# Kernel optimization log

Hardware: AMD Instinct MI355X
Metric: run time of the kernel (lower is better)

## Reference

```python
import jax, jax.numpy as jnp
import numpy as np

N_Q = 16384; N_S = 16384; NN = 32; F_IN = 128; F_OUT = 256
K = 15; DIM = 3
RADIUS = 10.0
KP_EXTENT_CFG = 1.0      # config.NETWORK.KP_EXTENT (also scales learned offsets)
DENSITY = 5.0            # config.NETWORK.DENSITY_PARAMETER
EXTENT = KP_EXTENT_CFG * RADIUS / DENSITY   # 2.0
K_RADIUS = 1.5 * EXTENT
OFFSET_DIM = DIM * (K - 1)  # modulated=False, version=0 -> 42


def setup_inputs() -> dict:
    key = jax.random.key(0)
    ks = jax.random.split(key, 8)
    query_points = jax.random.uniform(ks[0], (N_Q, DIM), dtype=jnp.float32)
    support_points = jax.random.uniform(ks[1], (N_S, DIM), dtype=jnp.float32)
    neighbors = jax.random.randint(ks[2], (N_Q, NN), 0, N_S)
    features = jax.random.normal(ks[3], (N_S, F_IN), dtype=jnp.float32)
    # kernel points: fixed disposition inside ball of radius 1.5*extent, first point at center
    kp = jax.random.normal(ks[4], (K, DIM), dtype=jnp.float32)
    kp = kp / jnp.linalg.norm(kp, axis=1, keepdims=True) * (0.7 * K_RADIUS)
    K_points = kp.at[0].set(0.0)
    weight = jax.random.normal(ks[5], (K, F_IN, F_OUT), dtype=jnp.float32) / np.sqrt(F_IN)
    deformable_weight = jax.random.normal(ks[6], (K, F_IN, OFFSET_DIM), dtype=jnp.float32) / np.sqrt(F_IN)
    bias = jnp.zeros((OFFSET_DIM,), dtype=jnp.float32)
    return {"query_points": query_points, "support_points": support_points,
            "neighbors": neighbors, "features": features, "K_points": K_points,
            "weight": weight, "deformable_weight": deformable_weight, "bias": bias}


def _gather_neighb(query_points, support_points, neighbors, features):
    # pad with shadow point (far away) and zero feature row, as in KPConv_ops
    sp = jnp.concatenate([support_points, jnp.full((1, DIM), 1e6, support_points.dtype)], 0)
    ft = jnp.concatenate([features, jnp.zeros((1, features.shape[1]), features.dtype)], 0)
    rel = sp[neighbors] - query_points[:, None, :]   # [n, nn, 3]
    nfeat = ft[neighbors]                            # [n, nn, f]
    return rel, nfeat


def _linear_influence(sq_dist):
    # KP_INFLUENCE='linear': relu(1 - d/extent); CONVOLUTION_MODE='sum'
    return jnp.maximum(1.0 - jnp.sqrt(sq_dist) / EXTENT, 0.0)


def reference(query_points, support_points, neighbors, features, K_points,
              weight, deformable_weight, bias):
    rel, nfeat = _gather_neighb(query_points, support_points, neighbors, features)

    # --- rigid KPConv producing offsets (version=0) ---
    d0 = rel[:, :, None, :] - K_points[None, None, :, :]   # [n, nn, K, 3]
    sq0 = jnp.sum(d0 * d0, axis=-1)                        # [n, nn, K]
    w0 = _linear_influence(sq0)
    wf0 = jnp.einsum('enk,enf->ekf', w0, nfeat)            # [n, K, f]
    feat0 = jnp.einsum('ekf,kfo->eo', wf0, deformable_weight) + bias  # [n, 42]

    # not modulated: reshape to offsets, prepend zero offset for center kernel point
    offsets = feat0.reshape(-1, K - 1, DIM)
    offsets = jnp.concatenate([jnp.zeros_like(offsets[:, :1, :]), offsets], axis=1)
    offsets = offsets * KP_EXTENT_CFG                      # [n, K, 3]

    # --- deformable KPConv ---
    def_kp = K_points[None, :, :] + offsets                # [n, K, 3]
    d1 = rel[:, :, None, :] - def_kp[:, None, :, :]        # [n, nn, K, 3]
    sq1 = jnp.sum(d1 * d1, axis=-1)                        # [n, nn, K]
    w1 = _linear_influence(sq1)                            # out-of-range neighbors get 0 weight
    wf1 = jnp.einsum('enk,enf->ekf', w1, nfeat)            # [n, K, f]
    out = jnp.einsum('ekf,kfo->eo', wf1, weight)           # [n, f_out]
    return out
```

## Files before the change

### kernel.cpp

```cpp
#include <hip/hip_runtime.h>
#include <hip/hip_bf16.h>
#include <math.h>

typedef __attribute__((ext_vector_type(8))) short bf16x8;
typedef __attribute__((ext_vector_type(4))) float f32x4;

#define NQ 16384
#define NN 32
#define FI 128
#define FO 256
#define KPN 15
#define OD 42
#define INV_EXT 0.5f

#define KT2 64
#define WST 2048

#define SWZ(row, blk) (((blk) ^ ((row) & 7)) << 5)

#define WS_FEATPK 0u
#define WS_BSW    (8u * 1024u * 1024u)
#define WS_DWBH   (9u * 1024u * 1024u)
#define WS_DWBL   (WS_DWBH + 196608u)
#define WS_DEFKP  (10u * 1024u * 1024u)

static __device__ __forceinline__ unsigned short f2bf(float x) {
    union { __hip_bfloat16 h; unsigned short u; } cv;
    cv.h = __float2bfloat16(x);
    return cv.u;
}
static __device__ __forceinline__ float bf2f(unsigned short h) {
    union { unsigned int u; float f; } cv;
    cv.u = ((unsigned int)h) << 16;
    return cv.f;
}

__global__ void pre_all(const float* __restrict__ feat, unsigned int* __restrict__ fpk,
                        const float* __restrict__ w, unsigned short* __restrict__ Bsw,
                        const float* __restrict__ dw,
                        unsigned short* __restrict__ dhi, unsigned short* __restrict__ dlo)
{
    const int b = blockIdx.x, t = threadIdx.x;
    if (b < 2048) {
        const int i = (b * 256 + t) * 4;
        float4 a = *(const float4*)&feat[i];
        unsigned short h0 = f2bf(a.x), h1 = f2bf(a.y), h2 = f2bf(a.z), h3 = f2bf(a.w);
        fpk[i + 0] = (unsigned int)h0 | ((unsigned int)f2bf(a.x - bf2f(h0)) << 16);
        fpk[i + 1] = (unsigned int)h1 | ((unsigned int)f2bf(a.y - bf2f(h1)) << 16);
        fpk[i + 2] = (unsigned int)h2 | ((unsigned int)f2bf(a.z - bf2f(h2)) << 16);
        fpk[i + 3] = (unsigned int)h3 | ((unsigned int)f2bf(a.w - bf2f(h3)) << 16);
    } else if (b < 2048 + 256) {
        const int tid = (b - 2048) * 256 + t;
        const int lane = tid & 63;
        const int kt   = (tid >> 6) & 63;
        const int nt   = tid >> 12;
        const int n    = nt * 16 + (lane & 15);
        const int kbase = kt * 32 + (lane >> 4) * 8;
        unsigned int p[4];
        #pragma unroll
        for (int jj = 0; jj < 4; jj++) {
            unsigned int lo, hi;
            {
                const int kk = kbase + 2 * jj;
                const int f = kk >> 4, k = kk & 15;
                lo = (k < KPN) ? f2bf(w[(k * FI + f) * FO + n]) : 0u;
            }
            {
                const int kk = kbase + 2 * jj + 1;
                const int f = kk >> 4, k = kk & 15;
                hi = (k < KPN) ? f2bf(w[(k * FI + f) * FO + n]) : 0u;
            }
            p[jj] = lo | (hi << 16);
        }
        unsigned int* op = (unsigned int*)&Bsw[tid * 8];
        op[0] = p[0]; op[1] = p[1]; op[2] = p[2]; op[3] = p[3];
    } else {
        const int tid = (b - 2304) * 256 + t;
        const int lane = tid & 63;
        const int kt   = (tid >> 6) & 63;
        const int nt   = tid >> 12;
        const int o    = nt * 16 + (lane & 15);
        const int kbase = kt * 32 + (lane >> 4) * 8;
        #pragma unroll
        for (int j = 0; j < 8; j++) {
            const int kf = kbase + j;
            const int f = kf >> 4, k = kf & 15;
            float v = (k < KPN && o < OD) ? dw[(k * FI + f) * OD + o] : 0.f;
            unsigned short h = f2bf(v);
            dhi[tid * 8 + j] = h;
            dlo[tid * 8 + j] = f2bf(v - bf2f(h));
        }
    }
}

__global__ __launch_bounds__(512, 4)
void k1_offsets(const float* __restrict__ query, const float* __restrict__ support,
                const int* __restrict__ neighbors, const unsigned int* __restrict__ featpk,
                const float* __restrict__ kpoints,
                const unsigned short* __restrict__ dwB_hi,
                const unsigned short* __restrict__ dwB_lo,
                const float* __restrict__ bias, float* __restrict__ defkp)
{
    __shared__ unsigned short wfA_hi[8 * WST];
    __shared__ unsigned short wfA_lo[8 * WST];
    __shared__ float relx[256], rely[256], relz[256];
    __shared__ int   nbr_s[256];
    __shared__ float kp_s[48];
    __shared__ f32x4 cred[3 * 64];

    const int t = threadIdx.x;
    const int qbase = blockIdx.x * 8;
    if (t < 45) kp_s[t] = kpoints[t];
    if (t >= 45 && t < 48) kp_s[t] = 0.f;

    if (t < 256) {
        const int e = t >> 5, n = t & 31;
        const int q = qbase + e;
        const int idx = neighbors[q * NN + n];
        nbr_s[t] = idx;
        relx[t] = support[idx * 3 + 0] - query[q * 3 + 0];
        rely[t] = support[idx * 3 + 1] - query[q * 3 + 1];
        relz[t] = support[idx * 3 + 2] - query[q * 3 + 2];
    }
    __syncthreads();

    const int wave = t >> 6, lane = t & 63;
    const int quad = lane >> 4, low = lane & 15;

    {
        const int ee = wave;
        const int kb = (low < KPN) ? low * 3 : 0;
        const float kx = kp_s[kb + 0], ky = kp_s[kb + 1], kz = kp_s[kb + 2];
        union { unsigned short u[8]; bf16x8 v; } ah, al;
        int rows[8];
        #pragma unroll
        for (int j = 0; j < 8; j++) {
            const int ni = ee * 32 + quad * 8 + j;
            rows[j] = nbr_s[ni];
            const float dx = relx[ni] - kx;
            const float dy = rely[ni] - ky;
            const float dz = relz[ni] - kz;
            const float d = sqrtf(dx * dx + dy * dy + dz * dz);
            float w = 1.0f - d * INV_EXT;
            w = (low < KPN && w > 0.f) ? w : 0.f;
            const unsigned short h = f2bf(w);
            ah.u[j] = h;
            al.u[j] = f2bf(w - bf2f(h));
        }
        #pragma unroll
        for (int ft = 0; ft < 8; ft++) {
            union { unsigned int u[4]; bf16x8 v; } bh, bl;
            #pragma unroll
            for (int jj = 0; jj < 4; jj++) {
                const unsigned int d0 = featpk[rows[2 * jj] * FI + ft * 16 + low];
                const unsigned int d1 = featpk[rows[2 * jj + 1] * FI + ft * 16 + low];
                bh.u[jj] = __builtin_amdgcn_perm(d1, d0, 0x05040100u);
                bl.u[jj] = __builtin_amdgcn_perm(d1, d0, 0x07060302u);
            }
            f32x4 acc = {0.f, 0.f, 0.f, 0.f};
            acc = __builtin_amdgcn_mfma_f32_16x16x32_bf16(al.v, bh.v, acc, 0, 0, 0);
            acc = __builtin_amdgcn_mfma_f32_16x16x32_bf16(ah.v, bl.v, acc, 0, 0, 0);
            acc = __builtin_amdgcn_mfma_f32_16x16x32_bf16(ah.v, bh.v, acc, 0, 0, 0);
            const int col  = ft * 16 + low;
            const int base = ee * WST + SWZ(ee, col >> 1) + ((col & 1) << 4) + quad * 4;
            const unsigned short h0 = f2bf(acc[0]), h1 = f2bf(acc[1]);
            const unsigned short h2 = f2bf(acc[2]), h3 = f2bf(acc[3]);
            unsigned int* ph = (unsigned int*)&wfA_hi[base];
            ph[0] = (unsigned int)h0 | ((unsigned int)h1 << 16);
            ph[1] = (unsigned int)h2 | ((unsigned int)h3 << 16);
            unsigned int* pl = (unsigned int*)&wfA_lo[base];
            pl[0] = (unsigned int)f2bf(acc[0] - bf2f(h0)) |
                    ((unsigned int)f2bf(acc[1] - bf2f(h1)) << 16);
            pl[1] = (unsigned int)f2bf(acc[2] - bf2f(h2)) |
                    ((unsigned int)f2bf(acc[3] - bf2f(h3)) << 16);
        }
    }
    __syncthreads();

    f32x4 acc = {0.f, 0.f, 0.f, 0.f};
    const int nt = wave >> 1, half = wave & 1;
    if (wave < 6) {
        const bf16x8* Bh = (const bf16x8*)dwB_hi;
        const bf16x8* Bl = (const bf16x8*)dwB_lo;
        const int rl = low & 7;
        const int arow = rl * WST;
        const int kt0 = half * 32;
        for (int kt = kt0; kt < kt0 + 32; kt++) {
            const int ao = arow + SWZ(rl, kt) + quad * 8;
            bf16x8 a_h = *(const bf16x8*)&wfA_hi[ao];
            bf16x8 a_l = *(const bf16x8*)&wfA_lo[ao];
            bf16x8 b_h = Bh[(nt * KT2 + kt) * 64 + lane];
            bf16x8 b_l = Bl[(nt * KT2 + kt) * 64 + lane];
            acc = __builtin_amdgcn_mfma_f32_16x16x32_bf16(a_l, b_h, acc, 0, 0, 0);
            acc = __builtin_amdgcn_mfma_f32_16x16x32_bf16(a_h, b_l, acc, 0, 0, 0);
            acc = __builtin_amdgcn_mfma_f32_16x16x32_bf16(a_h, b_h, acc, 0, 0, 0);
        }
        if (half == 1) cred[nt * 64 + lane] = acc;
    } else if (wave == 6 && lane < 24) {
        defkp[(qbase + lane / 3) * 45 + (lane % 3)] = kp_s[lane % 3];
    }
    __syncthreads();

    if (wave < 6 && half == 0) {
        f32x4 o2 = cred[nt * 64 + lane];
        acc[0] += o2[0]; acc[1] += o2[1]; acc[2] += o2[2]; acc[3] += o2[3];
        const int o = nt * 16 + low;
        if (quad < 2 && o < OD) {
            const float bo = bias[o] + kp_s[3 + o];
            #pragma unroll
            for (int r = 0; r < 4; r++) {
                const int ee = quad * 4 + r;
                defkp[(qbase + ee) * 45 + 3 + o] = bo + acc[r];
            }
        }
    }
}

__global__ __launch_bounds__(512, 4)
void k2_deform(const float* __restrict__ query, const float* __restrict__ support,
               const int* __restrict__ neighbors, const unsigned int* __restrict__ featpk,
               const unsigned short* __restrict__ Bsw, const float* __restrict__ defkp,
               float* __restrict__ out)
{
    __shared__ unsigned short wfA[16 * WST];
    __shared__ float relx[512], rely[512], relz[512];
    __shared__ float dk_s[16 * 45];
    __shared__ int   nbr_s[512];

    const int t = threadIdx.x;
    const int qbase = blockIdx.x * 16;

    for (int i = t; i < 16 * 45; i += 512) dk_s[i] = defkp[qbase * 45 + i];

    const int e = t >> 5, n = t & 31;
    const int q = qbase + e;
    const int idx = neighbors[q * NN + n];
    nbr_s[t] = idx;
    relx[t] = support[idx * 3 + 0] - query[q * 3 + 0];
    rely[t] = support[idx * 3 + 1] - query[q * 3 + 1];
    relz[t] = support[idx * 3 + 2] - query[q * 3 + 2];
    __syncthreads();

    const int wave = t >> 6, lane = t & 63;
    const int quad = lane >> 4, low = lane & 15;

    {
        const int kb = (low < KPN) ? low * 3 : 0;
        for (int ei = 0; ei < 2; ei++) {
            const int ee = wave * 2 + ei;
            const float kx = dk_s[ee * 45 + kb + 0];
            const float ky = dk_s[ee * 45 + kb + 1];
            const float kz = dk_s[ee * 45 + kb + 2];
            union { unsigned short u[8]; bf16x8 v; } a;
            int rows[8];
            #pragma unroll
            for (int j = 0; j < 8; j++) {
                const int ni = ee * 32 + quad * 8 + j;
                rows[j] = nbr_s[ni];
                const float dx = relx[ni] - kx;
                const float dy = rely[ni] - ky;
                const float dz = relz[ni] - kz;
                const float d = sqrtf(dx * dx + dy * dy + dz * dz);
                float w = 1.0f - d * INV_EXT;
                w = (low < KPN && w > 0.f) ? w : 0.f;
                a.u[j] = f2bf(w);
            }
            #pragma unroll
            for (int ft = 0; ft < 8; ft++) {
                union { unsigned int u[4]; bf16x8 v; } b;
                #pragma unroll
                for (int jj = 0; jj < 4; jj++) {
                    const unsigned int d0 = featpk[rows[2 * jj] * FI + ft * 16 + low];
                    const unsigned int d1 = featpk[rows[2 * jj + 1] * FI + ft * 16 + low];
                    b.u[jj] = __builtin_amdgcn_perm(d1, d0, 0x05040100u);
                }
                f32x4 acc = {0.f, 0.f, 0.f, 0.f};
                acc = __builtin_amdgcn_mfma_f32_16x16x32_bf16(a.v, b.v, acc, 0, 0, 0);
                const int col  = ft * 16 + low;
                const int base = ee * WST + SWZ(ee, col >> 1) + ((col & 1) << 4) + quad * 4;
                unsigned int* wp = (unsigned int*)&wfA[base];
                wp[0] = (unsigned int)f2bf(acc[0]) | ((unsigned int)f2bf(acc[1]) << 16);
                wp[1] = (unsigned int)f2bf(acc[2]) | ((unsigned int)f2bf(acc[3]) << 16);
            }
        }
    }
    __syncthreads();

    {
        const int nt0 = wave * 2, nt1 = nt0 + 1;
        f32x4 acc0 = {0.f, 0.f, 0.f, 0.f}, acc1 = {0.f, 0.f, 0.f, 0.f};
        const bf16x8* Bp = (const bf16x8*)Bsw;
        const int arow = low * WST;
        bf16x8 a_c  = *(const bf16x8*)&wfA[arow + SWZ(low, 0) + quad * 8];
        bf16x8 b0_c = Bp[(nt0 * KT2) * 64 + lane];
        bf16x8 b1_c = Bp[(nt1 * KT2) * 64 + lane];
        for (int kt = 0; kt < KT2 - 1; kt++) {
            bf16x8 a_n  = *(const bf16x8*)&wfA[arow + SWZ(low, kt + 1) + quad * 8];
            bf16x8 b0_n = Bp[(nt0 * KT2 + kt + 1) * 64 + lane];
            bf16x8 b1_n = Bp[(nt1 * KT2 + kt + 1) * 64 + lane];
            acc0 = __builtin_amdgcn_mfma_f32_16x16x32_bf16(a_c, b0_c, acc0, 0, 0, 0);
            acc1 = __builtin_amdgcn_mfma_f32_16x16x32_bf16(a_c, b1_c, acc1, 0, 0, 0);
            a_c = a_n; b0_c = b0_n; b1_c = b1_n;
        }
        acc0 = __builtin_amdgcn_mfma_f32_16x16x32_bf16(a_c, b0_c, acc0, 0, 0, 0);
        acc1 = __builtin_amdgcn_mfma_f32_16x16x32_bf16(a_c, b1_c, acc1, 0, 0, 0);
        #pragma unroll
        for (int r = 0; r < 4; r++) {
            const int ee = quad * 4 + r;
            out[(qbase + ee) * FO + nt0 * 16 + low] = acc0[r];
            out[(qbase + ee) * FO + nt1 * 16 + low] = acc1[r];
        }
    }
}

extern "C" void kernel_launch(void* const* d_in, const int* in_sizes, int n_in,
                              void* d_out, int out_size, void* d_ws, size_t ws_size,
                              hipStream_t stream) {
    const float* query     = (const float*)d_in[0];
    const float* support   = (const float*)d_in[1];
    const int*   neighbors = (const int*)  d_in[2];
    const float* features  = (const float*)d_in[3];
    const float* kpoints   = (const float*)d_in[4];
    const float* weight    = (const float*)d_in[5];
    const float* dweight   = (const float*)d_in[6];
    const float* bias      = (const float*)d_in[7];
    float*       out       = (float*)d_out;

    char* ws = (char*)d_ws;
    unsigned int*   featpk = (unsigned int*)(ws + WS_FEATPK);
    unsigned short* Bsw    = (unsigned short*)(ws + WS_BSW);
    unsigned short* dwBh   = (unsigned short*)(ws + WS_DWBH);
    unsigned short* dwBl   = (unsigned short*)(ws + WS_DWBL);
    float*          defkp  = (float*)(ws + WS_DEFKP);

    pre_all<<<2352, 256, 0, stream>>>(features, featpk, weight, Bsw,
                                      dweight, dwBh, dwBl);
    k1_offsets<<<NQ / 8, 512, 0, stream>>>(query, support, neighbors, featpk,
                                           kpoints, dwBh, dwBl, bias, defkp);
    k2_deform<<<NQ / 16, 512, 0, stream>>>(query, support, neighbors, featpk,
                                           Bsw, defkp, out);
}
```

Before: 197.2 us.

## Split feature packing into hi/lo and hi-only layouts with wider gathers

The preprocessing now writes two separate packed feature layouts. One interleaves hi/lo bf16 pairs so the offset kernel can fetch two feature columns with a single 8-byte load. The other holds only the hi bf16 values, so the deform kernel reads half the bytes per gathered row and gets two columns per 4-byte load. The dense GEMM loops also drop manual software pipelining in favour of compiler unroll pragmas. This trades extra workspace and a larger preprocessing launch for fewer, wider and smaller gather loads in the main kernels.

```diff
diff --git a/kernel.cpp b/kernel.cpp
--- a/kernel.cpp
+++ b/kernel.cpp
@@ -18,11 +18,12 @@
 
 #define SWZ(row, blk) (((blk) ^ ((row) & 7)) << 5)
 
-#define WS_FEATPK 0u
-#define WS_BSW    (8u * 1024u * 1024u)
-#define WS_DWBH   (9u * 1024u * 1024u)
+#define WS_FP1    0u
+#define WS_FP2    (8u * 1024u * 1024u)
+#define WS_BSW    (12u * 1024u * 1024u)
+#define WS_DWBH   (13u * 1024u * 1024u)
 #define WS_DWBL   (WS_DWBH + 196608u)
-#define WS_DEFKP  (10u * 1024u * 1024u)
+#define WS_DEFKP  (14u * 1024u * 1024u)
 
 static __device__ __forceinline__ unsigned short f2bf(float x) {
     union { __hip_bfloat16 h; unsigned short u; } cv;
@@ -35,22 +36,28 @@
     return cv.f;
 }
 
-__global__ void pre_all(const float* __restrict__ feat, unsigned int* __restrict__ fpk,
+__global__ void pre_all(const float* __restrict__ feat,
+                        unsigned int* __restrict__ fp1, unsigned int* __restrict__ fp2,
                         const float* __restrict__ w, unsigned short* __restrict__ Bsw,
                         const float* __restrict__ dw,
                         unsigned short* __restrict__ dhi, unsigned short* __restrict__ dlo)
 {
     const int b = blockIdx.x, t = threadIdx.x;
-    if (b < 2048) {
-        const int i = (b * 256 + t) * 4;
-        float4 a = *(const float4*)&feat[i];
-        unsigned short h0 = f2bf(a.x), h1 = f2bf(a.y), h2 = f2bf(a.z), h3 = f2bf(a.w);
-        fpk[i + 0] = (unsigned int)h0 | ((unsigned int)f2bf(a.x - bf2f(h0)) << 16);
-        fpk[i + 1] = (unsigned int)h1 | ((unsigned int)f2bf(a.y - bf2f(h1)) << 16);
-        fpk[i + 2] = (unsigned int)h2 | ((unsigned int)f2bf(a.z - bf2f(h2)) << 16);
-        fpk[i + 3] = (unsigned int)h3 | ((unsigned int)f2bf(a.w - bf2f(h3)) << 16);
-    } else if (b < 2048 + 256) {
-        const int tid = (b - 2048) * 256 + t;
+    if (b < 4096) {
+        const int tid = b * 256 + t;
+        const int s = tid >> 6, r = tid & 63;
+        const int fp = r >> 4, low = r & 15;
+        const float a = feat[s * FI + fp * 32 + low];
+        const float c = feat[s * FI + fp * 32 + 16 + low];
+        const unsigned short ha = f2bf(a), hc = f2bf(c);
+        const unsigned int w0 = (unsigned int)ha | ((unsigned int)hc << 16);
+        const unsigned int w1 = (unsigned int)f2bf(a - bf2f(ha)) |
+                                ((unsigned int)f2bf(c - bf2f(hc)) << 16);
+        uint2 pr; pr.x = w0; pr.y = w1;
+        *(uint2*)&fp1[s * 128 + fp * 32 + low * 2] = pr;
+        fp2[s * 64 + fp * 16 + low] = w0;
+    } else if (b < 4096 + 256) {
+        const int tid = (b - 4096) * 256 + t;
         const int lane = tid & 63;
         const int kt   = (tid >> 6) & 63;
         const int nt   = tid >> 12;
@@ -75,7 +82,7 @@
         unsigned int* op = (unsigned int*)&Bsw[tid * 8];
         op[0] = p[0]; op[1] = p[1]; op[2] = p[2]; op[3] = p[3];
     } else {
-        const int tid = (b - 2304) * 256 + t;
+        const int tid = (b - 4352) * 256 + t;
         const int lane = tid & 63;
         const int kt   = (tid >> 6) & 63;
         const int nt   = tid >> 12;
@@ -95,7 +102,7 @@
 
 __global__ __launch_bounds__(512, 4)
 void k1_offsets(const float* __restrict__ query, const float* __restrict__ support,
-                const int* __restrict__ neighbors, const unsigned int* __restrict__ featpk,
+                const int* __restrict__ neighbors, const unsigned int* __restrict__ fp1,
                 const float* __restrict__ kpoints,
                 const unsigned short* __restrict__ dwB_hi,
                 const unsigned short* __restrict__ dwB_lo,
@@ -148,31 +155,39 @@
             al.u[j] = f2bf(w - bf2f(h));
         }
         #pragma unroll
-        for (int ft = 0; ft < 8; ft++) {
-            union { unsigned int u[4]; bf16x8 v; } bh, bl;
+        for (int fp = 0; fp < 4; fp++) {
+            union { unsigned int u[4]; bf16x8 v; } bhA, blA, bhB, blB;
             #pragma unroll
             for (int jj = 0; jj < 4; jj++) {
-                const unsigned int d0 = featpk[rows[2 * jj] * FI + ft * 16 + low];
-                const unsigned int d1 = featpk[rows[2 * jj + 1] * FI + ft * 16 + low];
-                bh.u[jj] = __builtin_amdgcn_perm(d1, d0, 0x05040100u);
-                bl.u[jj] = __builtin_amdgcn_perm(d1, d0, 0x07060302u);
-            }
-            f32x4 acc = {0.f, 0.f, 0.f, 0.f};
-            acc = __builtin_amdgcn_mfma_f32_16x16x32_bf16(al.v, bh.v, acc, 0, 0, 0);
-            acc = __builtin_amdgcn_mfma_f32_16x16x32_bf16(ah.v, bl.v, acc, 0, 0, 0);
-            acc = __builtin_amdgcn_mfma_f32_16x16x32_bf16(ah.v, bh.v, acc, 0, 0, 0);
-            const int col  = ft * 16 + low;
-            const int base = ee * WST + SWZ(ee, col >> 1) + ((col & 1) << 4) + quad * 4;
-            const unsigned short h0 = f2bf(acc[0]), h1 = f2bf(acc[1]);
-            const unsigned short h2 = f2bf(acc[2]), h3 = f2bf(acc[3]);
-            unsigned int* ph = (unsigned int*)&wfA_hi[base];
-            ph[0] = (unsigned int)h0 | ((unsigned int)h1 << 16);
-            ph[1] = (unsigned int)h2 | ((unsigned int)h3 << 16);
-            unsigned int* pl = (unsigned int*)&wfA_lo[base];
-            pl[0] = (unsigned int)f2bf(acc[0] - bf2f(h0)) |
-                    ((unsigned int)f2bf(acc[1] - bf2f(h1)) << 16);
-            pl[1] = (unsigned int)f2bf(acc[2] - bf2f(h2)) |
-                    ((unsigned int)f2bf(acc[3] - bf2f(h3)) << 16);
+                const uint2 d0 = *(const uint2*)&fp1[rows[2 * jj] * 128 + fp * 32 + low * 2];
+                const uint2 d1 = *(const uint2*)&fp1[rows[2 * jj + 1] * 128 + fp * 32 + low * 2];
+                bhA.u[jj] = __builtin_amdgcn_perm(d1.x, d0.x, 0x05040100u);
+                bhB.u[jj] = __builtin_amdgcn_perm(d1.x, d0.x, 0x07060302u);
+                blA.u[jj] = __builtin_amdgcn_perm(d1.y, d0.y, 0x05040100u);
+                blB.u[jj] = __builtin_amdgcn_perm(d1.y, d0.y, 0x07060302u);
+            }
+            #pragma unroll
+            for (int hh2 = 0; hh2 < 2; hh2++) {
+                const bf16x8 bh = hh2 ? bhB.v : bhA.v;
+                const bf16x8 bl = hh2 ? blB.v : blA.v;
+                const int ft = fp * 2 + hh2;
+                f32x4 acc = {0.f, 0.f, 0.f, 0.f};
+                acc = __builtin_amdgcn_mfma_f32_16x16x32_bf16(al.v, bh, acc, 0, 0, 0);
+                acc = __builtin_amdgcn_mfma_f32_16x16x32_bf16(ah.v, bl, acc, 0, 0, 0);
+                acc = __builtin_amdgcn_mfma_f32_16x16x32_bf16(ah.v, bh, acc, 0, 0, 0);
+                const int col  = ft * 16 + low;
+                const int base = ee * WST + SWZ(ee, col >> 1) + ((col & 1) << 4) + quad * 4;
+                const unsigned short h0 = f2bf(acc[0]), h1 = f2bf(acc[1]);
+                const unsigned short h2 = f2bf(acc[2]), h3 = f2bf(acc[3]);
+                unsigned int* ph = (unsigned int*)&wfA_hi[base];
+                ph[0] = (unsigned int)h0 | ((unsigned int)h1 << 16);
+                ph[1] = (unsigned int)h2 | ((unsigned int)h3 << 16);
+                unsigned int* pl = (unsigned int*)&wfA_lo[base];
+                pl[0] = (unsigned int)f2bf(acc[0] - bf2f(h0)) |
+                        ((unsigned int)f2bf(acc[1] - bf2f(h1)) << 16);
+                pl[1] = (unsigned int)f2bf(acc[2] - bf2f(h2)) |
+                        ((unsigned int)f2bf(acc[3] - bf2f(h3)) << 16);
+            }
         }
     }
     __syncthreads();
@@ -185,6 +200,7 @@
         const int rl = low & 7;
         const int arow = rl * WST;
         const int kt0 = half * 32;
+        #pragma unroll 2
         for (int kt = kt0; kt < kt0 + 32; kt++) {
             const int ao = arow + SWZ(rl, kt) + quad * 8;
             bf16x8 a_h = *(const bf16x8*)&wfA_hi[ao];
@@ -218,7 +234,7 @@
 
 __global__ __launch_bounds__(512, 4)
 void k2_deform(const float* __restrict__ query, const float* __restrict__ support,
-               const int* __restrict__ neighbors, const unsigned int* __restrict__ featpk,
+               const int* __restrict__ neighbors, const unsigned int* __restrict__ fp2,
                const unsigned short* __restrict__ Bsw, const float* __restrict__ defkp,
                float* __restrict__ out)
 {
@@ -266,21 +282,27 @@
                 a.u[j] = f2bf(w);
             }
             #pragma unroll
-            for (int ft = 0; ft < 8; ft++) {
-                union { unsigned int u[4]; bf16x8 v; } b;
+            for (int fp = 0; fp < 4; fp++) {
+                union { unsigned int u[4]; bf16x8 v; } bA, bB;
                 #pragma unroll
                 for (int jj = 0; jj < 4; jj++) {
-                    const unsigned int d0 = featpk[rows[2 * jj] * FI + ft * 16 + low];
-                    const unsigned int d1 = featpk[rows[2 * jj + 1] * FI + ft * 16 + low];
-                    b.u[jj] = __builtin_amdgcn_perm(d1, d0, 0x05040100u);
+                    const unsigned int d0 = fp2[rows[2 * jj] * 64 + fp * 16 + low];
+                    const unsigned int d1 = fp2[rows[2 * jj + 1] * 64 + fp * 16 + low];
+                    bA.u[jj] = __builtin_amdgcn_perm(d1, d0, 0x05040100u);
+                    bB.u[jj] = __builtin_amdgcn_perm(d1, d0, 0x07060302u);
                 }
-                f32x4 acc = {0.f, 0.f, 0.f, 0.f};
-                acc = __builtin_amdgcn_mfma_f32_16x16x32_bf16(a.v, b.v, acc, 0, 0, 0);
-                const int col  = ft * 16 + low;
-                const int base = ee * WST + SWZ(ee, col >> 1) + ((col & 1) << 4) + quad * 4;
-                unsigned int* wp = (unsigned int*)&wfA[base];
-                wp[0] = (unsigned int)f2bf(acc[0]) | ((unsigned int)f2bf(acc[1]) << 16);
-                wp[1] = (unsigned int)f2bf(acc[2]) | ((unsigned int)f2bf(acc[3]) << 16);
+                #pragma unroll
+                for (int hh2 = 0; hh2 < 2; hh2++) {
+                    const bf16x8 b = hh2 ? bB.v : bA.v;
+                    const int ft = fp * 2 + hh2;
+                    f32x4 acc = {0.f, 0.f, 0.f, 0.f};
+                    acc = __builtin_amdgcn_mfma_f32_16x16x32_bf16(a.v, b, acc, 0, 0, 0);
+                    const int col  = ft * 16 + low;
+                    const int base = ee * WST + SWZ(ee, col >> 1) + ((col & 1) << 4) + quad * 4;
+                    unsigned int* wp = (unsigned int*)&wfA[base];
+                    wp[0] = (unsigned int)f2bf(acc[0]) | ((unsigned int)f2bf(acc[1]) << 16);
+                    wp[1] = (unsigned int)f2bf(acc[2]) | ((unsigned int)f2bf(acc[3]) << 16);
+                }
             }
         }
     }
@@ -291,19 +313,14 @@
         f32x4 acc0 = {0.f, 0.f, 0.f, 0.f}, acc1 = {0.f, 0.f, 0.f, 0.f};
         const bf16x8* Bp = (const bf16x8*)Bsw;
         const int arow = low * WST;
-        bf16x8 a_c  = *(const bf16x8*)&wfA[arow + SWZ(low, 0) + quad * 8];
-        bf16x8 b0_c = Bp[(nt0 * KT2) * 64 + lane];
-        bf16x8 b1_c = Bp[(nt1 * KT2) * 64 + lane];
-        for (int kt = 0; kt < KT2 - 1; kt++) {
-            bf16x8 a_n  = *(const bf16x8*)&wfA[arow + SWZ(low, kt + 1) + quad * 8];
-            bf16x8 b0_n = Bp[(nt0 * KT2 + kt + 1) * 64 + lane];
-            bf16x8 b1_n = Bp[(nt1 * KT2 + kt + 1) * 64 + lane];
-            acc0 = __builtin_amdgcn_mfma_f32_16x16x32_bf16(a_c, b0_c, acc0, 0, 0, 0);
-            acc1 = __builtin_amdgcn_mfma_f32_16x16x32_bf16(a_c, b1_c, acc1, 0, 0, 0);
-            a_c = a_n; b0_c = b0_n; b1_c = b1_n;
-        }
-        acc0 = __builtin_amdgcn_mfma_f32_16x16x32_bf16(a_c, b0_c, acc0, 0, 0, 0);
-        acc1 = __builtin_amdgcn_mfma_f32_16x16x32_bf16(a_c, b1_c, acc1, 0, 0, 0);
+        #pragma unroll 4
+        for (int kt = 0; kt < KT2; kt++) {
+            bf16x8 a  = *(const bf16x8*)&wfA[arow + SWZ(low, kt) + quad * 8];
+            bf16x8 b0 = Bp[(nt0 * KT2 + kt) * 64 + lane];
+            bf16x8 b1 = Bp[(nt1 * KT2 + kt) * 64 + lane];
+            acc0 = __builtin_amdgcn_mfma_f32_16x16x32_bf16(a, b0, acc0, 0, 0, 0);
+            acc1 = __builtin_amdgcn_mfma_f32_16x16x32_bf16(a, b1, acc1, 0, 0, 0);
+        }
         #pragma unroll
         for (int r = 0; r < 4; r++) {
             const int ee = quad * 4 + r;
@@ -327,16 +344,17 @@
     float*       out       = (float*)d_out;
 
     char* ws = (char*)d_ws;
-    unsigned int*   featpk = (unsigned int*)(ws + WS_FEATPK);
-    unsigned short* Bsw    = (unsigned short*)(ws + WS_BSW);
-    unsigned short* dwBh   = (unsigned short*)(ws + WS_DWBH);
-    unsigned short* dwBl   = (unsigned short*)(ws + WS_DWBL);
-    float*          defkp  = (float*)(ws + WS_DEFKP);
-
-    pre_all<<<2352, 256, 0, stream>>>(features, featpk, weight, Bsw,
+    unsigned int*   fp1  = (unsigned int*)(ws + WS_FP1);
+    unsigned int*   fp2  = (unsigned int*)(ws + WS_FP2);
+    unsigned short* Bsw  = (unsigned short*)(ws + WS_BSW);
+    unsigned short* dwBh = (unsigned short*)(ws + WS_DWBH);
+    unsigned short* dwBl = (unsigned short*)(ws + WS_DWBL);
+    float*          defkp = (float*)(ws + WS_DEFKP);
+
+    pre_all<<<4400, 256, 0, stream>>>(features, fp1, fp2, weight, Bsw,
                                       dweight, dwBh, dwBl);
-    k1_offsets<<<NQ / 8, 512, 0, stream>>>(query, support, neighbors, featpk,
+    k1_offsets<<<NQ / 8, 512, 0, stream>>>(query, support, neighbors, fp1,
                                            kpoints, dwBh, dwBl, bias, defkp);
-    k2_deform<<<NQ / 16, 512, 0, stream>>>(query, support, neighbors, featpk,
+    k2_deform<<<NQ / 16, 512, 0, stream>>>(query, support, neighbors, fp2,
                                            Bsw, defkp, out);
 }
```

Result: faster. 191.0 us (-3.1%).
